# Performance work log

Hardware: AMD Instinct MI355X
Metric: run time of the kernel (lower is better)

Reference implementation:

```python
import jax, jax.numpy as jnp
import numpy as np

H = 16            # num heads
D_NOPE = 128
D_ROPE = 64
D_V = 128
Q_LORA = 1536
KV_LORA = 512
HIDDEN = 2048
EPS = 1e-6


def rmsnorm(x, w):
    xf = x.astype(jnp.float32)
    var = jnp.mean(xf * xf, axis=-1, keepdims=True)
    return (w * (xf * jax.lax.rsqrt(var + EPS))).astype(x.dtype)


def rope_interleaved(x, cos, sin):
    # x: [B,H,S,D]; cos,sin: [S,D] -> use even-index entries as the per-pair values
    B, nH, S, D = x.shape
    cv = cos[:, 0::2].astype(jnp.float32)[None, None]  # [1,1,S,D/2]
    sv = sin[:, 0::2].astype(jnp.float32)[None, None]
    xf = x.astype(jnp.float32).reshape(B, nH, S, D // 2, 2)
    xr, xi = xf[..., 0], xf[..., 1]
    out = jnp.stack([xr * cv - xi * sv, xr * sv + xi * cv], axis=-1)
    return out.reshape(B, nH, S, D).astype(x.dtype)


def setup_inputs() -> dict:
    key = jax.random.key(0)
    ks = jax.random.split(key, 9)
    B, S = 2, 2048
    std = 0.02
    return {
        "hidden_states": jax.random.normal(ks[0], (B, S, HIDDEN), jnp.float32),
        "cos": jax.random.uniform(ks[1], (S, D_ROPE), jnp.float32),
        "sin": jax.random.uniform(ks[2], (S, D_ROPE), jnp.float32),
        "q_a_w": jax.random.normal(ks[3], (HIDDEN, Q_LORA), jnp.float32) * std,
        "q_a_ln_w": jnp.ones((Q_LORA,), jnp.float32),
        "q_b_w": jax.random.normal(ks[4], (Q_LORA, H * (D_NOPE + D_ROPE)), jnp.float32) * std,
        "kv_a_w": jax.random.normal(ks[5], (HIDDEN, KV_LORA + D_ROPE), jnp.float32) * std,
        "kv_a_ln_w": jnp.ones((KV_LORA,), jnp.float32),
        "kv_b_w": jax.random.normal(ks[6], (KV_LORA, H * (D_NOPE + D_V)), jnp.float32) * std,
        "o_w": jax.random.normal(ks[7], (H * D_V, HIDDEN), jnp.float32) * std,
    }


def reference(hidden_states, cos, sin, q_a_w, q_a_ln_w, q_b_w, kv_a_w, kv_a_ln_w, kv_b_w, o_w):
    B, S, _ = hidden_states.shape
    scale = 1.0 / np.sqrt(D_NOPE + D_ROPE)

    # Q path: low-rank down-proj, RMSNorm, up-proj
    q = rmsnorm(hidden_states @ q_a_w, q_a_ln_w) @ q_b_w
    q = q.reshape(B, S, H, D_NOPE + D_ROPE).transpose(0, 2, 1, 3)  # [B,H,S,Dq]
    q_nope, q_rope = q[..., :D_NOPE], q[..., D_NOPE:]

    # KV path: compressed kv + shared rope key
    ckv = hidden_states @ kv_a_w  # [B,S,KV_LORA+D_ROPE]
    compressed_kv, k_rope = ckv[..., :KV_LORA], ckv[..., KV_LORA:]
    k_rope = jnp.broadcast_to(k_rope[:, None], (B, H, S, D_ROPE))
    kv = rmsnorm(compressed_kv, kv_a_ln_w) @ kv_b_w
    kv = kv.reshape(B, S, H, D_NOPE + D_V).transpose(0, 2, 1, 3)  # [B,H,S,Dk+Dv]
    k_nope, value = kv[..., :D_NOPE], kv[..., D_NOPE:]

    q_rope = rope_interleaved(q_rope, cos, sin)
    k_rope = rope_interleaved(k_rope, cos, sin)

    query = jnp.concatenate([q_nope, q_rope], axis=-1)  # [B,H,S,192]
    key = jnp.concatenate([k_nope, k_rope], axis=-1)

    attn = jnp.einsum("bhqd,bhkd->bhqk", query, key) * scale
    attn = jax.nn.softmax(attn.astype(jnp.float32), axis=-1).astype(query.dtype)
    out = jnp.einsum("bhqk,bhkd->bhqd", attn, value)  # [B,H,S,Dv]
    out = out.transpose(0, 2, 1, 3).reshape(B, S, H * D_V)
    return out @ o_w
```

## Files before the change

### kernel.cpp

```cpp
#include <hip/hip_runtime.h>

typedef unsigned short u16;
typedef __bf16 bf16x8 __attribute__((ext_vector_type(8)));
typedef float f32x4 __attribute__((ext_vector_type(4)));

#define S_ 2048

__device__ __forceinline__ u16 f2bf(float f) {
  union { float f; unsigned u; } v; v.f = f;
  unsigned r = v.u + 0x7fffu + ((v.u >> 16) & 1u);
  return (u16)(r >> 16);
}
__device__ __forceinline__ float bf2f(u16 h) {
  union { unsigned u; float f; } v; v.u = ((unsigned)h) << 16;
  return v.f;
}

__device__ __forceinline__ f32x4 mfma16(bf16x8 a, bf16x8 b, f32x4 c) {
  return __builtin_amdgcn_mfma_f32_16x16x32_bf16(a, b, c, 0, 0, 0);
}

__device__ __forceinline__ void async16(const void* g, void* l) {
  __builtin_amdgcn_global_load_lds((__attribute__((address_space(1))) void*)g,
                                   (__attribute__((address_space(3))) void*)l,
                                   16, 0, 0);
}

__global__ void cast_bf_k(const float* __restrict__ in, u16* __restrict__ out, int n) {
  int i = blockIdx.x * 256 + threadIdx.x;
  if (i < n) out[i] = f2bf(in[i]);
}

__global__ void transw_k(const float* __restrict__ W, u16* __restrict__ Wt,
                         int K, int N, int Npad) {
  __shared__ float tile[32][33];
  int k0 = blockIdx.x * 32, n0 = blockIdx.y * 32;
  int tx = threadIdx.x, ty = threadIdx.y;
#pragma unroll
  for (int r = 0; r < 32; r += 8) {
    int n = n0 + tx;
    tile[ty + r][tx] = (n < N) ? W[(long)(k0 + ty + r) * N + n] : 0.f;
  }
  __syncthreads();
#pragma unroll
  for (int r = 0; r < 32; r += 8) {
    Wt[(long)(n0 + ty + r) * K + k0 + tx] = f2bf(tile[tx][ty + r]);
  }
}

template <typename OUT_T>
__global__ __launch_bounds__(256)
void gemm_bt_k(const u16* __restrict__ A, const u16* __restrict__ Bt,
               OUT_T* __restrict__ C, int K, int Nc, int ldc) {
  __shared__ __align__(16) u16 sA[128 * 32];
  __shared__ __align__(16) u16 sB[128 * 32];
  int tid = threadIdx.x;
  int lane = tid & 63, w = tid >> 6;
  int wr = w >> 1, wc = w & 1;
  int l15 = lane & 15, quad = lane >> 4;
  long tm = (long)blockIdx.y * 128;
  long tn = (long)blockIdx.x * 128;
  const u16* Ab = A + tm * K;
  const u16* Bb = Bt + tn * K;
  f32x4 acc[4][4] = {};

  for (int k0 = 0; k0 < K; k0 += 32) {
#pragma unroll
    for (int it = 0; it < 2; ++it) {
      int c = tid + it * 256;
      int row = c >> 2, kc = c & 3;
      async16(Ab + (long)row * K + k0 + kc * 8, sA + c * 8);
      async16(Bb + (long)row * K + k0 + kc * 8, sB + c * 8);
    }
    __syncthreads();
    bf16x8 af[4], bfr[4];
#pragma unroll
    for (int i = 0; i < 4; ++i)
      af[i] = *(const bf16x8*)(sA + (wr * 64 + i * 16 + l15) * 32 + quad * 8);
#pragma unroll
    for (int j = 0; j < 4; ++j)
      bfr[j] = *(const bf16x8*)(sB + (wc * 64 + j * 16 + l15) * 32 + quad * 8);
#pragma unroll
    for (int i = 0; i < 4; ++i)
#pragma unroll
      for (int j = 0; j < 4; ++j)
        acc[i][j] = mfma16(af[i], bfr[j], acc[i][j]);
    __syncthreads();
  }
#pragma unroll
  for (int i = 0; i < 4; ++i) {
#pragma unroll
    for (int j = 0; j < 4; ++j) {
      int col = (int)tn + wc * 64 + j * 16 + l15;
      if (col < Nc) {
#pragma unroll
        for (int r = 0; r < 4; ++r) {
          long row = tm + wr * 64 + i * 16 + quad * 4 + r;
          float v = acc[i][j][r];
          if constexpr (sizeof(OUT_T) == 2) C[row * ldc + col] = f2bf(v);
          else                              C[row * ldc + col] = v;
        }
      }
    }
  }
}

__global__ __launch_bounds__(256)
void rmsnorm_k(const float* __restrict__ in, int ld, int N,
               const float* __restrict__ w, u16* __restrict__ out, int ldo) {
  int row = blockIdx.x;
  const float* x = in + (long)row * ld;
  float ss = 0.f;
  for (int i = threadIdx.x; i < N; i += 256) { float v = x[i]; ss += v * v; }
#pragma unroll
  for (int off = 32; off; off >>= 1) ss += __shfl_down(ss, off);
  __shared__ float red[4];
  if ((threadIdx.x & 63) == 0) red[threadIdx.x >> 6] = ss;
  __syncthreads();
  float inv = rsqrtf((red[0] + red[1] + red[2] + red[3]) / N + 1e-6f);
  u16* o = out + (long)row * ldo;
  for (int i = threadIdx.x; i < N; i += 256) o[i] = f2bf(w[i] * x[i] * inv);
}

__global__ void krope_k(const float* __restrict__ ckv, const float* __restrict__ cs,
                        const float* __restrict__ sn, u16* __restrict__ out) {
  int idx = blockIdx.x * 256 + threadIdx.x;
  int row = idx >> 5, i = idx & 31;
  int s = row & (S_ - 1);
  float xr = ckv[(long)row * 576 + 512 + 2 * i];
  float xi = ckv[(long)row * 576 + 512 + 2 * i + 1];
  float cv = cs[s * 64 + 2 * i], sv = sn[s * 64 + 2 * i];
  out[(long)row * 64 + 2 * i]     = f2bf(xr * cv - xi * sv);
  out[(long)row * 64 + 2 * i + 1] = f2bf(xr * sv + xi * cv);
}

__global__ void qrope_k(u16* __restrict__ qb, const float* __restrict__ cs,
                        const float* __restrict__ sn) {
  int idx = blockIdx.x * 256 + threadIdx.x;
  int row = idx >> 9;
  int rem = idx & 511, h = rem >> 5, i = rem & 31;
  int s = row & (S_ - 1);
  long base = (long)row * 3072 + h * 192 + 128 + 2 * i;
  float xr = bf2f(qb[base]), xi = bf2f(qb[base + 1]);
  float cv = cs[s * 64 + 2 * i], sv = sn[s * 64 + 2 * i];
  qb[base]     = f2bf(xr * cv - xi * sv);
  qb[base + 1] = f2bf(xr * sv + xi * cv);
}

__global__ void transv_k(const u16* __restrict__ kvb, u16* __restrict__ vt) {
  int bh = blockIdx.z, b = bh >> 4, h = bh & 15;
  const u16* src = kvb + (long)b * S_ * 4096 + h * 256 + 128;
  u16* dst = vt + (long)bh * 128 * 2048;
  __shared__ u16 tile[32][33];
  int s0 = blockIdx.x * 32, d0 = blockIdx.y * 32;
  int tx = threadIdx.x, ty = threadIdx.y;
#pragma unroll
  for (int r = 0; r < 32; r += 8)
    tile[ty + r][tx] = src[(long)(s0 + ty + r) * 4096 + d0 + tx];
  __syncthreads();
#pragma unroll
  for (int r = 0; r < 32; r += 8)
    dst[(long)(d0 + ty + r) * 2048 + s0 + tx] = tile[tx][ty + r];
}

__global__ void kswz_k(const u16* __restrict__ kvb, const u16* __restrict__ kr,
                       u16* __restrict__ kswz) {
  int tile = blockIdx.x;
  int bh = tile >> 5, kt = tile & 31;
  int b = bh >> 4, h = bh & 15;
  u16* dst = kswz + (long)tile * 12288;
#pragma unroll
  for (int i = 0; i < 6; ++i) {
    int c = threadIdx.x + i * 256;
    int frag = c >> 6, lane = c & 63;
    int kg = frag / 6, db = frag % 6;
    int key = kt * 64 + kg * 16 + (lane & 15);
    int d = db * 32 + (lane >> 4) * 8;
    const u16* src;
    if (d < 128) src = kvb + ((long)(b * S_ + key)) * 4096 + h * 256 + d;
    else         src = kr  + ((long)(b * S_ + key)) * 64 + (d - 128);
    *(f32x4*)(dst + c * 8) = *(const f32x4*)src;
  }
}

__global__ void vswz_k(const u16* __restrict__ vt, u16* __restrict__ vswz) {
  int tile = blockIdx.x;
  int bh = tile >> 5, kt = tile & 31;
  u16* dst = vswz + (long)tile * 8192;
  const u16* src0 = vt + (long)bh * 128 * 2048;
#pragma unroll
  for (int i = 0; i < 4; ++i) {
    int c = threadIdx.x + i * 256;
    int frag = c >> 6, lane = c & 63;
    int kq = frag >> 3, j = frag & 7;
    int d = j * 16 + (lane & 15);
    int key = kt * 64 + kq * 32 + (lane >> 4) * 8;
    *(f32x4*)(dst + c * 8) = *(const f32x4*)(src0 + (long)d * 2048 + key);
  }
}

__global__ __launch_bounds__(256, 2)
void attn_k(const u16* __restrict__ qb, const u16* __restrict__ kswz,
            const u16* __restrict__ vswz, u16* __restrict__ attnO) {
  int bh = blockIdx.y, b = bh >> 4, h = bh & 15;
  int qt = blockIdx.x;
  int tid = threadIdx.x, lane = tid & 63, w = tid >> 6;
  int l15 = lane & 15, quad = lane >> 4;
  int qrow0 = qt * 128 + w * 32;

  __shared__ __align__(16) u16 sK[24 * 64 * 8];
  __shared__ __align__(16) u16 sV[16 * 64 * 8];
  __shared__ __align__(16) u16 pT[4][32 * 72];

  bf16x8 qf[2][6];
#pragma unroll
  for (int rg = 0; rg < 2; ++rg) {
    const u16* qp = qb + ((long)(b * S_ + qrow0 + rg * 16 + l15)) * 3072 + h * 192 + quad * 8;
#pragma unroll
    for (int kb = 0; kb < 6; ++kb) qf[rg][kb] = *(const bf16x8*)(qp + kb * 32);
  }

  f32x4 o[2][8] = {};
  float lsum[2][4] = {};
  u16* pw = pT[w];
  const float scale = 0.07216878364870322f;

#pragma unroll 1
  for (int kt = 0; kt < 32; ++kt) {
    const u16* Kt = kswz + ((long)bh * 32 + kt) * 12288;
    const u16* Vt = vswz + ((long)bh * 32 + kt) * 8192;
    __syncthreads();
#pragma unroll
    for (int i = 0; i < 6; ++i) {
      int c = tid + i * 256;
      async16(Kt + c * 8, sK + c * 8);
    }
#pragma unroll
    for (int i = 0; i < 4; ++i) {
      int c = tid + i * 256;
      async16(Vt + c * 8, sV + c * 8);
    }
    __syncthreads();

    f32x4 s[2][4] = {};
#pragma unroll
    for (int kg = 0; kg < 4; ++kg) {
#pragma unroll
      for (int db = 0; db < 6; ++db) {
        bf16x8 kf = *(const bf16x8*)(sK + ((kg * 6 + db) * 64 + lane) * 8);
        s[0][kg] = mfma16(qf[0][db], kf, s[0][kg]);
        s[1][kg] = mfma16(qf[1][db], kf, s[1][kg]);
      }
    }
#pragma unroll
    for (int rg = 0; rg < 2; ++rg) {
#pragma unroll
      for (int kg = 0; kg < 4; ++kg) {
#pragma unroll
        for (int r = 0; r < 4; ++r) {
          float p = __expf(s[rg][kg][r] * scale);
          lsum[rg][r] += p;
          pw[(rg * 16 + quad * 4 + r) * 72 + kg * 16 + l15] = f2bf(p);
        }
      }
    }
#pragma unroll
    for (int kq = 0; kq < 2; ++kq) {
      bf16x8 pf0 = *(const bf16x8*)(pw + (l15) * 72 + kq * 32 + quad * 8);
      bf16x8 pf1 = *(const bf16x8*)(pw + (16 + l15) * 72 + kq * 32 + quad * 8);
#pragma unroll
      for (int j = 0; j < 8; ++j) {
        bf16x8 vf = *(const bf16x8*)(sV + ((kq * 8 + j) * 64 + lane) * 8);
        o[0][j] = mfma16(pf0, vf, o[0][j]);
        o[1][j] = mfma16(pf1, vf, o[1][j]);
      }
    }
  }

  float inv[2][4];
#pragma unroll
  for (int rg = 0; rg < 2; ++rg)
#pragma unroll
    for (int r = 0; r < 4; ++r) {
      float s = lsum[rg][r];
#pragma unroll
      for (int off = 8; off; off >>= 1) s += __shfl_xor(s, off);
      inv[rg][r] = 1.f / s;
    }
#pragma unroll
  for (int rg = 0; rg < 2; ++rg) {
    u16* op = attnO + ((long)(b * S_ + qrow0 + rg * 16)) * 2048 + h * 128;
#pragma unroll
    for (int j = 0; j < 8; ++j)
#pragma unroll
      for (int r = 0; r < 4; ++r)
        op[(long)(quad * 4 + r) * 2048 + j * 16 + l15] = f2bf(o[rg][j][r] * inv[rg][r]);
  }
}

extern "C" void kernel_launch(void* const* d_in, const int* in_sizes, int n_in,
                              void* d_out, int out_size, void* d_ws, size_t ws_size,
                              hipStream_t stream) {
  const float* hs      = (const float*)d_in[0];
  const float* cosb    = (const float*)d_in[1];
  const float* sinb    = (const float*)d_in[2];
  const float* q_a_w   = (const float*)d_in[3];
  const float* q_a_ln  = (const float*)d_in[4];
  const float* q_b_w   = (const float*)d_in[5];
  const float* kv_a_w  = (const float*)d_in[6];
  const float* kv_a_ln = (const float*)d_in[7];
  const float* kv_b_w  = (const float*)d_in[8];
  const float* o_w     = (const float*)d_in[9];
  float* out = (float*)d_out;
  (void)in_sizes; (void)n_in; (void)out_size; (void)ws_size;

  char* p = (char*)d_ws;
  auto alloc = [&](size_t b) { char* r = p; p += (b + 255) & ~((size_t)255); return r; };
  u16*   hs_bf = (u16*)  alloc((size_t)4096 * 2048 * 2);
  u16*   qawT  = (u16*)  alloc((size_t)1536 * 2048 * 2);
  u16*   kvawT = (u16*)  alloc((size_t)640  * 2048 * 2);
  u16*   qbwT  = (u16*)  alloc((size_t)3072 * 1536 * 2);
  u16*   kvbwT = (u16*)  alloc((size_t)4096 * 512  * 2);
  u16*   owT   = (u16*)  alloc((size_t)2048 * 2048 * 2);
  float* qa    = (float*)alloc((size_t)4096 * 1536 * 4);
  u16*   qan   = (u16*)  alloc((size_t)4096 * 1536 * 2);
  float* ckv   = (float*)alloc((size_t)4096 * 576  * 4);
  u16*   ckvn  = (u16*)  alloc((size_t)4096 * 512  * 2);
  u16*   kr    = (u16*)  alloc((size_t)4096 * 64   * 2);
  u16*   qbuf  = (u16*)  alloc((size_t)4096 * 3072 * 2);
  u16*   kvbuf = (u16*)  alloc((size_t)4096 * 4096 * 2);
  u16*   vtb   = (u16*)  alloc((size_t)32 * 128 * 2048 * 2);
  u16*   aO    = (u16*)  alloc((size_t)4096 * 2048 * 2);
  u16* kswz = (u16*)qa;
  u16* vswz = (u16*)hs_bf;

  dim3 tb(32, 8);
  cast_bf_k<<<32768, 256, 0, stream>>>(hs, hs_bf, 4096 * 2048);
  transw_k<<<dim3(64, 48),  tb, 0, stream>>>(q_a_w,  qawT,  2048, 1536, 1536);
  transw_k<<<dim3(64, 20),  tb, 0, stream>>>(kv_a_w, kvawT, 2048, 576,  640);
  transw_k<<<dim3(48, 96),  tb, 0, stream>>>(q_b_w,  qbwT,  1536, 3072, 3072);
  transw_k<<<dim3(16, 128), tb, 0, stream>>>(kv_b_w, kvbwT, 512,  4096, 4096);
  transw_k<<<dim3(64, 64),  tb, 0, stream>>>(o_w,    owT,   2048, 2048, 2048);

  gemm_bt_k<float><<<dim3(12, 32), 256, 0, stream>>>(hs_bf, qawT,  qa,  2048, 1536, 1536);
  gemm_bt_k<float><<<dim3(5, 32),  256, 0, stream>>>(hs_bf, kvawT, ckv, 2048, 576,  576);
  rmsnorm_k<<<4096, 256, 0, stream>>>(qa,  1536, 1536, q_a_ln,  qan,  1536);
  rmsnorm_k<<<4096, 256, 0, stream>>>(ckv, 576,  512,  kv_a_ln, ckvn, 512);
  krope_k<<<512, 256, 0, stream>>>(ckv, cosb, sinb, kr);
  gemm_bt_k<u16><<<dim3(24, 32), 256, 0, stream>>>(qan,  qbwT,  qbuf,  1536, 3072, 3072);
  qrope_k<<<8192, 256, 0, stream>>>(qbuf, cosb, sinb);
  gemm_bt_k<u16><<<dim3(32, 32), 256, 0, stream>>>(ckvn, kvbwT, kvbuf, 512,  4096, 4096);
  transv_k<<<dim3(64, 4, 32), tb, 0, stream>>>(kvbuf, vtb);
  kswz_k<<<1024, 256, 0, stream>>>(kvbuf, kr, kswz);
  vswz_k<<<1024, 256, 0, stream>>>(vtb, vswz);
  attn_k<<<dim3(16, 32), 256, 0, stream>>>(qbuf, kswz, vswz, aO);
  gemm_bt_k<float><<<dim3(16, 32), 256, 0, stream>>>(aO, owT, out, 2048, 2048, 2048);
}
```

Measured before the change: 547.4 us.

## Fuse Q/KV down-projections, fold q-rope into GEMM epilogue, merge V transpose-swizzle

Concatenates the q_a and kv_a weight transposes so one GEMM produces both down-projections, removing a separate small GEMM launch with poor tile utilization. Applies interleaved RoPE to the query rope columns inside the q_b GEMM epilogue using a lane shuffle with the pair partner, eliminating the qrope read-modify-write pass. Replaces the V transpose plus swizzle with a single LDS-staged kernel that reads kvbuf directly, dropping the intermediate vt buffer. The epilogue now does extra modulo, shuffle and cos/sin loads per element, and the padded rows of the fused GEMM output are no longer needed.

After: 518.5 us. 5.3% less time.

```diff
diff --git a/kernel.cpp b/kernel.cpp
--- a/kernel.cpp
+++ b/kernel.cpp
@@ -32,7 +32,7 @@
 }
 
 __global__ void transw_k(const float* __restrict__ W, u16* __restrict__ Wt,
-                         int K, int N, int Npad) {
+                         int K, int N) {
   __shared__ float tile[32][33];
   int k0 = blockIdx.x * 32, n0 = blockIdx.y * 32;
   int tx = threadIdx.x, ty = threadIdx.y;
@@ -48,10 +48,11 @@
   }
 }
 
-template <typename OUT_T>
+template <typename OUT_T, bool ROPE>
 __global__ __launch_bounds__(256)
 void gemm_bt_k(const u16* __restrict__ A, const u16* __restrict__ Bt,
-               OUT_T* __restrict__ C, int K, int Nc, int ldc) {
+               OUT_T* __restrict__ C, int K, int Nc, int ldc,
+               const float* __restrict__ cs, const float* __restrict__ sn) {
   __shared__ __align__(16) u16 sA[128 * 32];
   __shared__ __align__(16) u16 sB[128 * 32];
   int tid = threadIdx.x;
@@ -93,10 +94,26 @@
     for (int j = 0; j < 4; ++j) {
       int col = (int)tn + wc * 64 + j * 16 + l15;
       if (col < Nc) {
+        bool ropeT = false;
+        int fi = 0;
+        if constexpr (ROPE) {
+          int d = col % 192;
+          ropeT = (d >= 128);
+          fi = (d - 128) & ~1;
+        }
 #pragma unroll
         for (int r = 0; r < 4; ++r) {
           long row = tm + wr * 64 + i * 16 + quad * 4 + r;
           float v = acc[i][j][r];
+          if constexpr (ROPE) {
+            float partner = __shfl_xor(v, 1);
+            if (ropeT) {
+              int si = (int)row & (S_ - 1);
+              float cv = cs[si * 64 + fi], sv = sn[si * 64 + fi];
+              v = (l15 & 1) ? (partner * sv + v * cv)
+                            : (v * cv - partner * sv);
+            }
+          }
           if constexpr (sizeof(OUT_T) == 2) C[row * ldc + col] = f2bf(v);
           else                              C[row * ldc + col] = v;
         }
@@ -122,45 +139,17 @@
   for (int i = threadIdx.x; i < N; i += 256) o[i] = f2bf(w[i] * x[i] * inv);
 }
 
-__global__ void krope_k(const float* __restrict__ ckv, const float* __restrict__ cs,
-                        const float* __restrict__ sn, u16* __restrict__ out) {
+__global__ void krope_k(const float* __restrict__ src, int ld,
+                        const float* __restrict__ cs, const float* __restrict__ sn,
+                        u16* __restrict__ out) {
   int idx = blockIdx.x * 256 + threadIdx.x;
   int row = idx >> 5, i = idx & 31;
   int s = row & (S_ - 1);
-  float xr = ckv[(long)row * 576 + 512 + 2 * i];
-  float xi = ckv[(long)row * 576 + 512 + 2 * i + 1];
+  float xr = src[(long)row * ld + 2 * i];
+  float xi = src[(long)row * ld + 2 * i + 1];
   float cv = cs[s * 64 + 2 * i], sv = sn[s * 64 + 2 * i];
   out[(long)row * 64 + 2 * i]     = f2bf(xr * cv - xi * sv);
   out[(long)row * 64 + 2 * i + 1] = f2bf(xr * sv + xi * cv);
-}
-
-__global__ void qrope_k(u16* __restrict__ qb, const float* __restrict__ cs,
-                        const float* __restrict__ sn) {
-  int idx = blockIdx.x * 256 + threadIdx.x;
-  int row = idx >> 9;
-  int rem = idx & 511, h = rem >> 5, i = rem & 31;
-  int s = row & (S_ - 1);
-  long base = (long)row * 3072 + h * 192 + 128 + 2 * i;
-  float xr = bf2f(qb[base]), xi = bf2f(qb[base + 1]);
-  float cv = cs[s * 64 + 2 * i], sv = sn[s * 64 + 2 * i];
-  qb[base]     = f2bf(xr * cv - xi * sv);
-  qb[base + 1] = f2bf(xr * sv + xi * cv);
-}
-
-__global__ void transv_k(const u16* __restrict__ kvb, u16* __restrict__ vt) {
-  int bh = blockIdx.z, b = bh >> 4, h = bh & 15;
-  const u16* src = kvb + (long)b * S_ * 4096 + h * 256 + 128;
-  u16* dst = vt + (long)bh * 128 * 2048;
-  __shared__ u16 tile[32][33];
-  int s0 = blockIdx.x * 32, d0 = blockIdx.y * 32;
-  int tx = threadIdx.x, ty = threadIdx.y;
-#pragma unroll
-  for (int r = 0; r < 32; r += 8)
-    tile[ty + r][tx] = src[(long)(s0 + ty + r) * 4096 + d0 + tx];
-  __syncthreads();
-#pragma unroll
-  for (int r = 0; r < 32; r += 8)
-    dst[(long)(d0 + ty + r) * 2048 + s0 + tx] = tile[tx][ty + r];
 }
 
 __global__ void kswz_k(const u16* __restrict__ kvb, const u16* __restrict__ kr,
@@ -183,19 +172,32 @@
   }
 }
 
-__global__ void vswz_k(const u16* __restrict__ vt, u16* __restrict__ vswz) {
+__global__ void vswz2_k(const u16* __restrict__ kvb, u16* __restrict__ vswz) {
   int tile = blockIdx.x;
   int bh = tile >> 5, kt = tile & 31;
+  int b = bh >> 4, h = bh & 15;
+  __shared__ __align__(16) u16 t[64 * 136];
+  int tid = threadIdx.x;
+#pragma unroll
+  for (int i = 0; i < 4; ++i) {
+    int c = tid + i * 256;
+    int row = c >> 4, dc = (c & 15) * 8;
+    *(f32x4*)(t + row * 136 + dc) =
+        *(const f32x4*)(kvb + ((long)(b * S_ + kt * 64 + row)) * 4096 + h * 256 + 128 + dc);
+  }
+  __syncthreads();
   u16* dst = vswz + (long)tile * 8192;
-  const u16* src0 = vt + (long)bh * 128 * 2048;
 #pragma unroll
   for (int i = 0; i < 4; ++i) {
-    int c = threadIdx.x + i * 256;
+    int c = tid + i * 256;
     int frag = c >> 6, lane = c & 63;
     int kq = frag >> 3, j = frag & 7;
     int d = j * 16 + (lane & 15);
-    int key = kt * 64 + kq * 32 + (lane >> 4) * 8;
-    *(f32x4*)(dst + c * 8) = *(const f32x4*)(src0 + (long)d * 2048 + key);
+    int keyl = kq * 32 + (lane >> 4) * 8;
+    union { u16 v[8]; f32x4 q; } u;
+#pragma unroll
+    for (int e = 0; e < 8; ++e) u.v[e] = t[(keyl + e) * 136 + d];
+    *(f32x4*)(dst + c * 8) = u.q;
   }
 }
 
@@ -316,43 +318,41 @@
 
   char* p = (char*)d_ws;
   auto alloc = [&](size_t b) { char* r = p; p += (b + 255) & ~((size_t)255); return r; };
-  u16*   hs_bf = (u16*)  alloc((size_t)4096 * 2048 * 2);
-  u16*   qawT  = (u16*)  alloc((size_t)1536 * 2048 * 2);
-  u16*   kvawT = (u16*)  alloc((size_t)640  * 2048 * 2);
-  u16*   qbwT  = (u16*)  alloc((size_t)3072 * 1536 * 2);
-  u16*   kvbwT = (u16*)  alloc((size_t)4096 * 512  * 2);
-  u16*   owT   = (u16*)  alloc((size_t)2048 * 2048 * 2);
-  float* qa    = (float*)alloc((size_t)4096 * 1536 * 4);
-  u16*   qan   = (u16*)  alloc((size_t)4096 * 1536 * 2);
-  float* ckv   = (float*)alloc((size_t)4096 * 576  * 4);
-  u16*   ckvn  = (u16*)  alloc((size_t)4096 * 512  * 2);
-  u16*   kr    = (u16*)  alloc((size_t)4096 * 64   * 2);
-  u16*   qbuf  = (u16*)  alloc((size_t)4096 * 3072 * 2);
-  u16*   kvbuf = (u16*)  alloc((size_t)4096 * 4096 * 2);
-  u16*   vtb   = (u16*)  alloc((size_t)32 * 128 * 2048 * 2);
-  u16*   aO    = (u16*)  alloc((size_t)4096 * 2048 * 2);
-  u16* kswz = (u16*)qa;
+  u16*   hs_bf  = (u16*)  alloc((size_t)4096 * 2048 * 2);
+  u16*   qakvT  = (u16*)  alloc((size_t)2176 * 2048 * 2);
+  u16*   qbwT   = (u16*)  alloc((size_t)3072 * 1536 * 2);
+  u16*   kvbwT  = (u16*)  alloc((size_t)4096 * 512  * 2);
+  u16*   owT    = (u16*)  alloc((size_t)2048 * 2048 * 2);
+  float* qa_ckv = (float*)alloc((size_t)4096 * 2176 * 4);
+  u16*   qan    = (u16*)  alloc((size_t)4096 * 1536 * 2);
+  u16*   ckvn   = (u16*)  alloc((size_t)4096 * 512  * 2);
+  u16*   kr     = (u16*)  alloc((size_t)4096 * 64   * 2);
+  u16*   qbuf   = (u16*)  alloc((size_t)4096 * 3072 * 2);
+  u16*   kvbuf  = (u16*)  alloc((size_t)4096 * 4096 * 2);
+  u16*   aO     = (u16*)  alloc((size_t)4096 * 2048 * 2);
+  u16* kswz = (u16*)qa_ckv;
   u16* vswz = (u16*)hs_bf;
 
   dim3 tb(32, 8);
   cast_bf_k<<<32768, 256, 0, stream>>>(hs, hs_bf, 4096 * 2048);
-  transw_k<<<dim3(64, 48),  tb, 0, stream>>>(q_a_w,  qawT,  2048, 1536, 1536);
-  transw_k<<<dim3(64, 20),  tb, 0, stream>>>(kv_a_w, kvawT, 2048, 576,  640);
-  transw_k<<<dim3(48, 96),  tb, 0, stream>>>(q_b_w,  qbwT,  1536, 3072, 3072);
-  transw_k<<<dim3(16, 128), tb, 0, stream>>>(kv_b_w, kvbwT, 512,  4096, 4096);
-  transw_k<<<dim3(64, 64),  tb, 0, stream>>>(o_w,    owT,   2048, 2048, 2048);
-
-  gemm_bt_k<float><<<dim3(12, 32), 256, 0, stream>>>(hs_bf, qawT,  qa,  2048, 1536, 1536);
-  gemm_bt_k<float><<<dim3(5, 32),  256, 0, stream>>>(hs_bf, kvawT, ckv, 2048, 576,  576);
-  rmsnorm_k<<<4096, 256, 0, stream>>>(qa,  1536, 1536, q_a_ln,  qan,  1536);
-  rmsnorm_k<<<4096, 256, 0, stream>>>(ckv, 576,  512,  kv_a_ln, ckvn, 512);
-  krope_k<<<512, 256, 0, stream>>>(ckv, cosb, sinb, kr);
-  gemm_bt_k<u16><<<dim3(24, 32), 256, 0, stream>>>(qan,  qbwT,  qbuf,  1536, 3072, 3072);
-  qrope_k<<<8192, 256, 0, stream>>>(qbuf, cosb, sinb);
-  gemm_bt_k<u16><<<dim3(32, 32), 256, 0, stream>>>(ckvn, kvbwT, kvbuf, 512,  4096, 4096);
-  transv_k<<<dim3(64, 4, 32), tb, 0, stream>>>(kvbuf, vtb);
+  transw_k<<<dim3(64, 48),  tb, 0, stream>>>(q_a_w,  qakvT,                     2048, 1536);
+  transw_k<<<dim3(64, 20),  tb, 0, stream>>>(kv_a_w, qakvT + (long)1536 * 2048, 2048, 576);
+  transw_k<<<dim3(48, 96),  tb, 0, stream>>>(q_b_w,  qbwT,  1536, 3072);
+  transw_k<<<dim3(16, 128), tb, 0, stream>>>(kv_b_w, kvbwT, 512,  4096);
+  transw_k<<<dim3(64, 64),  tb, 0, stream>>>(o_w,    owT,   2048, 2048);
+
+  gemm_bt_k<float, false><<<dim3(17, 32), 256, 0, stream>>>(
+      hs_bf, qakvT, qa_ckv, 2048, 2176, 2176, nullptr, nullptr);
+  rmsnorm_k<<<4096, 256, 0, stream>>>(qa_ckv,        2176, 1536, q_a_ln,  qan,  1536);
+  rmsnorm_k<<<4096, 256, 0, stream>>>(qa_ckv + 1536, 2176, 512,  kv_a_ln, ckvn, 512);
+  krope_k<<<512, 256, 0, stream>>>(qa_ckv + 2048, 2176, cosb, sinb, kr);
+  gemm_bt_k<u16, true><<<dim3(24, 32), 256, 0, stream>>>(
+      qan, qbwT, qbuf, 1536, 3072, 3072, cosb, sinb);
+  gemm_bt_k<u16, false><<<dim3(32, 32), 256, 0, stream>>>(
+      ckvn, kvbwT, kvbuf, 512, 4096, 4096, nullptr, nullptr);
   kswz_k<<<1024, 256, 0, stream>>>(kvbuf, kr, kswz);
-  vswz_k<<<1024, 256, 0, stream>>>(vtb, vswz);
+  vswz2_k<<<1024, 256, 0, stream>>>(kvbuf, vswz);
   attn_k<<<dim3(16, 32), 256, 0, stream>>>(qbuf, kswz, vswz, aO);
-  gemm_bt_k<float><<<dim3(16, 32), 256, 0, stream>>>(aO, owT, out, 2048, 2048, 2048);
-}
+  gemm_bt_k<float, false><<<dim3(16, 32), 256, 0, stream>>>(
+      aO, owT, out, 2048, 2048, 2048, nullptr, nullptr);
+}
```
